# Kernel optimization log

Measured on AMD Instinct MI355X. Metric: run time of the kernel, lower is better.

## Reference

```python
import jax, jax.numpy as jnp
import numpy as np

N, T, D, E1 = 64, 32, 128, 128
EPS = 1e-6


def _mlp(x, W1, b1, W2, b2):
    # Linear -> ReLU -> (Dropout: identity in eval) -> Linear
    return jnp.maximum(x @ W1 + b1, 0.0) @ W2 + b2


def _forward(x_time, x_news,
             it_W1, it_b1, it_W2, it_b2,
             inw_W1, inw_b1, inw_W2, inw_b2,
             t2n_W1, t2n_b1, t2n_W2, t2n_b2,
             n2t_W1, n2t_b1, n2t_W2, n2t_b2,
             f_W1, f_b1, f_W2, f_b2,
             theta_t, theta_n):
    xt = x_time.reshape(-1, D)   # [NT, D]
    xn = x_news.reshape(-1, D)   # [NT, D]

    # incidence-matrix candidates, each [NT, E1]
    H_time = xt @ _mlp(xt.T, it_W1, it_b1, it_W2, it_b2)
    H_news = xn @ _mlp(xn.T, inw_W1, inw_b1, inw_W2, inw_b2)
    H_t2n = xt @ _mlp(xn.T, t2n_W1, t2n_b1, t2n_W2, t2n_b2)
    H_n2t = xn @ _mlp(xt.T, n2t_W1, n2t_b1, n2t_W2, n2t_b2)

    H = _mlp(jnp.concatenate([H_time, H_news, H_t2n, H_n2t], axis=1),
             f_W1, f_b1, f_W2, f_b2)  # [NT, E1]

    # column-wise standardization (torch.std is unbiased -> ddof=1) + softmax over nodes
    H = (H - H.mean(axis=0, keepdims=True)) / (H.std(axis=0, ddof=1, keepdims=True) + EPS)
    H = jax.nn.softmax(H, axis=0)

    # pairwise Jensen-Shannon divergence between columns of H -> [E1, E1]
    logH = jnp.log(H)
    M = (H[:, :, None] + H[:, None, :]) * 0.5          # [NT, E1, E1]
    kl_pm = jnp.sum(H[:, :, None] * (logH[:, :, None] - jnp.log(M)), axis=0)  # KL(P||M)
    # KL(Q||M)[i,j] == KL(P||M)[j,i] since M is symmetric in (i,j)
    jsd = (kl_pm + kl_pm.T) * 0.5

    jm = jsd.mean(axis=0)                               # [E1]
    njm = (jm - jm.mean()) / (jm.std(ddof=1) + EPS)
    w = jax.nn.softmax(njm)                             # diagonal of hyperedge weight W

    # Hypergraph conv with residual: x + elu(H @ diag(w) @ H.T @ x @ theta)
    # reassociated (exactly equal math) to avoid the O((NT)^2) intermediate
    Hw = H * w[None, :]                                 # [NT, E1]
    xt = xt + jax.nn.elu(Hw @ (H.T @ (xt @ theta_t)))
    xn = xn + jax.nn.elu(Hw @ (H.T @ (xn @ theta_n)))

    return xt.reshape(N, T, D), xn.reshape(N, T, D)


def setup_inputs() -> dict:
    key = jax.random.key(0)
    ks = iter(jax.random.split(key, 32))
    NT = N * T

    def lin(i, o):
        return (jax.random.normal(next(ks), (i, o), jnp.float32) / np.float32(np.sqrt(i)))

    inp = {
        "x_time": jax.random.normal(next(ks), (N, T, D), jnp.float32),
        "x_news": jax.random.normal(next(ks), (N, T, D), jnp.float32),
    }
    for pre in ["it", "inw", "t2n", "n2t"]:
        inp[pre + "_W1"] = lin(NT, E1)
        inp[pre + "_b1"] = jnp.zeros((E1,), jnp.float32)
        inp[pre + "_W2"] = lin(E1, E1)
        inp[pre + "_b2"] = jnp.zeros((E1,), jnp.float32)
    inp["f_W1"] = lin(4 * E1, E1)
    inp["f_b1"] = jnp.zeros((E1,), jnp.float32)
    inp["f_W2"] = lin(E1, E1)
    inp["f_b2"] = jnp.zeros((E1,), jnp.float32)
    # HypergraphConvolution uses torch.randn init for theta
    inp["theta_t"] = jax.random.normal(next(ks), (D, D), jnp.float32)
    inp["theta_n"] = jax.random.normal(next(ks), (D, D), jnp.float32)
    return inp


def reference(x_time, x_news,
              it_W1, it_b1, it_W2, it_b2,
              inw_W1, inw_b1, inw_W2, inw_b2,
              t2n_W1, t2n_b1, t2n_W2, t2n_b2,
              n2t_W1, n2t_b1, n2t_W2, n2t_b2,
              f_W1, f_b1, f_W2, f_b2,
              theta_t, theta_n):
    return _forward(x_time, x_news,
                    it_W1, it_b1, it_W2, it_b2,
                    inw_W1, inw_b1, inw_W2, inw_b2,
                    t2n_W1, t2n_b1, t2n_W2, t2n_b2,
                    n2t_W1, n2t_b1, n2t_W2, n2t_b2,
                    f_W1, f_b1, f_W2, f_b2,
                    theta_t, theta_n)
```

## Files before the change

kernel.cpp:

```cpp
#include <hip/hip_runtime.h>
#include <hip/hip_bf16.h>
#include <math.h>

#define NTOT 2048
#define DIM  128
#define MSPLIT 16
#define ZSPLIT 16
#define JT 16
#define JNC 128
#define JNSPLIT 16

struct P4 { const float* p[4]; };

__global__ __launch_bounds__(256) void gk_mlp1t(P4 X, P4 W1, float* __restrict__ Gs) {
  int k = blockIdx.z;
  int m0 = (blockIdx.x & 3) * 32;
  int e0 = (blockIdx.x >> 2) * 32;
  int split = blockIdx.y;
  int n0 = split * (NTOT / MSPLIT);
  const float* Xp = X.p[k];
  const float* Wp = W1.p[k];
  __shared__ float Xs[32][36], Ws[32][36];
  int tid = threadIdx.x;
  int lr = tid >> 3;
  int lc = (tid & 7) * 4;
  int tx = tid & 15, ty = tid >> 4;
  float a00 = 0.f, a01 = 0.f, a10 = 0.f, a11 = 0.f;
  long g0 = (long)(n0 + lr) * DIM;
  float4 xv = *(const float4*)(Xp + g0 + m0 + lc);
  float4 wv = *(const float4*)(Wp + g0 + e0 + lc);
  for (int nb = 0; nb < NTOT / MSPLIT; nb += 32) {
    *(float4*)&Xs[lr][lc] = xv;
    *(float4*)&Ws[lr][lc] = wv;
    __syncthreads();
    if (nb + 32 < NTOT / MSPLIT) {
      long gn = (long)(n0 + nb + 32 + lr) * DIM;
      xv = *(const float4*)(Xp + gn + m0 + lc);
      wv = *(const float4*)(Wp + gn + e0 + lc);
    }
    #pragma unroll
    for (int nn = 0; nn < 32; ++nn) {
      float x0 = Xs[nn][2*ty], x1 = Xs[nn][2*ty+1];
      float w0 = Ws[nn][2*tx], w1 = Ws[nn][2*tx+1];
      a00 += x0 * w0; a01 += x0 * w1;
      a10 += x1 * w0; a11 += x1 * w1;
    }
    __syncthreads();
  }
  float* Gk = Gs + ((long)k * MSPLIT + split) * 16384;
  int m = m0 + 2 * ty, e = e0 + 2 * tx;
  Gk[m * DIM + e]           = a00;
  Gk[m * DIM + e + 1]       = a01;
  Gk[(m + 1) * DIM + e]     = a10;
  Gk[(m + 1) * DIM + e + 1] = a11;
}

__global__ __launch_bounds__(256) void gk_mab(const float* __restrict__ Gs, P4 B1, P4 W2, P4 B2,
                                              const float* __restrict__ fW1, float* __restrict__ AB) {
  int m = blockIdx.x;
  int e = threadIdx.x & 127;
  int half = threadIdx.x >> 7;
  int k0 = half, k1 = half + 2;
  __shared__ float rk[4][DIM];
  __shared__ float mk[4][DIM];
  {
    const float* G0 = Gs + (long)k0 * MSPLIT * 16384 + m * DIM + e;
    const float* G1 = Gs + (long)k1 * MSPLIT * 16384 + m * DIM + e;
    float s0 = 0.f, s1 = 0.f;
    #pragma unroll
    for (int s = 0; s < MSPLIT; ++s) { s0 += G0[s * 16384]; s1 += G1[s * 16384]; }
    rk[k0][e] = fmaxf(s0 + B1.p[k0][e], 0.f);
    rk[k1][e] = fmaxf(s1 + B1.p[k1][e], 0.f);
  }
  __syncthreads();
  {
    const float* Wa = W2.p[k0];
    const float* Wb = W2.p[k1];
    float a0 = B2.p[k0][e], a1 = B2.p[k1][e];
    #pragma unroll 8
    for (int j = 0; j < DIM; ++j) {
      a0 += rk[k0][j] * Wa[j * DIM + e];
      a1 += rk[k1][j] * Wb[j * DIM + e];
    }
    mk[k0][e] = a0;
    mk[k1][e] = a1;
  }
  __syncthreads();
  const float* Ma = mk[half];
  const float* Mb = mk[half + 2];
  const float* W0 = fW1 + (half == 0 ? 0 : 128) * DIM;
  const float* W1p = fW1 + (half == 0 ? 256 : 384) * DIM;
  float acc = 0.f;
  #pragma unroll 8
  for (int j = 0; j < DIM; ++j)
    acc += Ma[j] * W0[j * DIM + e] + Mb[j] * W1p[j * DIM + e];
  AB[(long)half * 16384 + m * DIM + e] = acc;
}

__global__ __launch_bounds__(256) void gk_h12t(const float* __restrict__ xt, const float* __restrict__ xn,
                                               const float* __restrict__ AB, const float* __restrict__ fb1,
                                               const float* __restrict__ fW2, const float* __restrict__ fb2,
                                               float* __restrict__ HrawT) {
  int n0 = blockIdx.x * 8;
  int e  = threadIdx.x & 127;
  int rr = (threadIdx.x >> 7) << 2;
  __shared__ float stT[DIM][8], snT[DIM][8], h1T[DIM][8];
  {
    int c = threadIdx.x & 31, rq = threadIdx.x >> 5;
    const float* xtr = xt + (long)(n0 + rq) * DIM;
    const float* xnr = xn + (long)(n0 + rq) * DIM;
    #pragma unroll
    for (int i = 0; i < 4; ++i) {
      int d = c + 32 * i;
      stT[d][rq] = xtr[d];
      snT[d][rq] = xnr[d];
    }
  }
  __syncthreads();
  float4 acc1 = make_float4(0.f, 0.f, 0.f, 0.f);
  #pragma unroll 8
  for (int k = 0; k < DIM; ++k) {
    float a = AB[k * DIM + e];
    float b = AB[16384 + k * DIM + e];
    const float4 xv = *(const float4*)&stT[k][rr];
    const float4 nv = *(const float4*)&snT[k][rr];
    acc1.x += xv.x * a + nv.x * b;
    acc1.y += xv.y * a + nv.y * b;
    acc1.z += xv.z * a + nv.z * b;
    acc1.w += xv.w * a + nv.w * b;
  }
  float b1v = fb1[e];
  float4 h1;
  h1.x = fmaxf(acc1.x + b1v, 0.f);
  h1.y = fmaxf(acc1.y + b1v, 0.f);
  h1.z = fmaxf(acc1.z + b1v, 0.f);
  h1.w = fmaxf(acc1.w + b1v, 0.f);
  *(float4*)&h1T[e][rr] = h1;
  __syncthreads();
  float4 acc2 = make_float4(0.f, 0.f, 0.f, 0.f);
  #pragma unroll 8
  for (int j = 0; j < DIM; ++j) {
    float wv = fW2[j * DIM + e];
    const float4 hv = *(const float4*)&h1T[j][rr];
    acc2.x += hv.x * wv;
    acc2.y += hv.y * wv;
    acc2.z += hv.z * wv;
    acc2.w += hv.w * wv;
  }
  float b2v = fb2[e];
  float4 o;
  o.x = acc2.x + b2v; o.y = acc2.y + b2v; o.z = acc2.z + b2v; o.w = acc2.w + b2v;
  *(float4*)&HrawT[(long)e * NTOT + n0 + rr] = o;
}

__global__ __launch_bounds__(256) void colsoft_k(const float* __restrict__ HrawT,
                                                 float* __restrict__ HTp, float* __restrict__ Ecol,
                                                 float* __restrict__ Gacc) {
  int e = blockIdx.x;
  int t = threadIdx.x;
  if (e == 0 && t < DIM) Gacc[t] = 0.f;
  __shared__ float sa[4], sb[4], sc[4];
  float v[8];
  float sum = 0.f, sq = 0.f, mx = -3.4e38f;
  #pragma unroll
  for (int r = 0; r < 8; ++r) {
    float x = HrawT[(long)e * NTOT + t + 256 * r];
    v[r] = x;
    sum += x; sq += x * x; mx = fmaxf(mx, x);
  }
  #pragma unroll
  for (int o = 32; o > 0; o >>= 1) {
    sum += __shfl_down(sum, o);
    sq  += __shfl_down(sq, o);
    mx   = fmaxf(mx, __shfl_down(mx, o));
  }
  if ((t & 63) == 0) { int w = t >> 6; sa[w] = sum; sb[w] = sq; sc[w] = mx; }
  __syncthreads();
  sum = sa[0] + sa[1] + sa[2] + sa[3];
  sq  = sb[0] + sb[1] + sb[2] + sb[3];
  mx  = fmaxf(fmaxf(sc[0], sc[1]), fmaxf(sc[2], sc[3]));
  float mean = sum * (1.f / NTOT);
  float var  = (sq - sum * mean) * (1.f / (NTOT - 1));
  float ia   = 1.f / (sqrtf(fmaxf(var, 0.f)) + 1e-6f);
  float smax = (mx - mean) * ia;
  __syncthreads();

  float den = 0.f;
  #pragma unroll
  for (int r = 0; r < 8; ++r) {
    float s = (v[r] - mean) * ia - smax;
    v[r] = s;
    den += __expf(s);
  }
  #pragma unroll
  for (int o = 32; o > 0; o >>= 1) den += __shfl_down(den, o);
  if ((t & 63) == 0) sa[t >> 6] = den;
  __syncthreads();
  den = sa[0] + sa[1] + sa[2] + sa[3];
  float logden = __logf(den);
  float invden = 1.f / den;
  __syncthreads();

  float ent = 0.f;
  #pragma unroll
  for (int r = 0; r < 8; ++r) {
    float s = v[r];
    float pv = __expf(s) * invden;
    HTp[(long)e * NTOT + t + 256 * r] = pv;
    ent += pv * (s - logden);
  }
  #pragma unroll
  for (int o = 32; o > 0; o >>= 1) ent += __shfl_down(ent, o);
  if ((t & 63) == 0) sa[t >> 6] = ent;
  __syncthreads();
  if (t == 0) Ecol[e] = sa[0] + sa[1] + sa[2] + sa[3];
}

__global__ __launch_bounds__(256) void jx_k(const float* __restrict__ HTp,
                                            const float* __restrict__ xt, const float* __restrict__ xn,
                                            float* __restrict__ g, float* __restrict__ Xzs) {
  __shared__ union {
    struct { float Ti[JT][JNC + 2], Tj[JT][JNC + 2], red[JT][JT + 1]; } j;
    struct { float As[32][33], Bs[32][36]; } x;
  } sm;
  int bid = blockIdx.x;
  int tid = threadIdx.x;

  if (bid < 576) {
    int ny = bid / 36, b = bid - ny * 36;
    int bi = 0, rem = b;
    while (rem >= 8 - bi) { rem -= 8 - bi; ++bi; }
    int bj = bi + rem;
    int n0 = ny * (NTOT / JNSPLIT);
    int ti = tid >> 4, tj = tid & 15;
    bool active = (bi != bj) || (ti < tj);
    int lc = tid >> 4, ln = (tid & 15) * 8;
    const float* si = HTp + (long)(bi * JT + lc) * NTOT + n0 + ln;
    const float* sj = HTp + (long)(bj * JT + lc) * NTOT + n0 + ln;
    #pragma unroll
    for (int r = 0; r < 8; ++r) sm.j.Ti[lc][ln + r] = si[r];
    #pragma unroll
    for (int r = 0; r < 8; ++r) sm.j.Tj[lc][ln + r] = sj[r];
    __syncthreads();
    float acc = 0.f;
    if (active) {
      #pragma unroll 4
      for (int n = 0; n < JNC; ++n) {
        float s = sm.j.Ti[ti][n] + sm.j.Tj[tj][n];
        acc += s * __logf(fmaxf(0.5f * s, 1e-38f));
      }
    }
    sm.j.red[ti][tj] = active ? acc : 0.f;
    __syncthreads();
    if (tid < JT) {
      float s = 0.f;
      #pragma unroll
      for (int q = 0; q < JT; ++q) s += sm.j.red[tid][q];
      atomicAdd(&g[bi * JT + tid], -s);
    } else if (tid < 2 * JT) {
      int c2 = tid - JT;
      float s = 0.f;
      #pragma unroll
      for (int i = 0; i < JT; ++i) s += sm.j.red[i][c2];
      atomicAdd(&g[bj * JT + c2], -s);
    }
  } else {
    int id = bid - 576;
    int bt = id >> 8;
    int split = (id >> 4) & 15;
    int t16 = id & 15;
    const float* x = bt ? xn : xt;
    float* C = Xzs + ((long)bt * ZSPLIT + split) * 16384;
    int e0 = (t16 & 3) * 32, d0 = (t16 >> 2) * 32;
    int n0 = split * (NTOT / ZSPLIT);
    int col = tid & 31, row = tid >> 5;
    int lr = tid >> 3, lc4 = (tid & 7) * 4;
    int tx = tid & 15, ty = tid >> 4;
    float a00 = 0.f, a01 = 0.f, a10 = 0.f, a11 = 0.f;
    float pa[4]; float4 pb;
    #pragma unroll
    for (int r = 0; r < 4; ++r) pa[r] = HTp[(long)(e0 + row + r * 8) * NTOT + n0 + col];
    pb = *(const float4*)(x + (long)(n0 + lr) * DIM + d0 + lc4);
    for (int nb = 0; nb < NTOT / ZSPLIT; nb += 32) {
      #pragma unroll
      for (int r = 0; r < 4; ++r) sm.x.As[col][row + r * 8] = pa[r];
      *(float4*)&sm.x.Bs[lr][lc4] = pb;
      __syncthreads();
      if (nb + 32 < NTOT / ZSPLIT) {
        #pragma unroll
        for (int r = 0; r < 4; ++r)
          pa[r] = HTp[(long)(e0 + row + r * 8) * NTOT + n0 + nb + 32 + col];
        pb = *(const float4*)(x + (long)(n0 + nb + 32 + lr) * DIM + d0 + lc4);
      }
      #pragma unroll
      for (int nn = 0; nn < 32; ++nn) {
        float e0v = sm.x.As[nn][2*ty], e1v = sm.x.As[nn][2*ty+1];
        float d0v = sm.x.Bs[nn][2*tx], d1v = sm.x.Bs[nn][2*tx+1];
        a00 += e0v * d0v; a01 += e0v * d1v;
        a10 += e1v * d0v; a11 += e1v * d1v;
      }
      __syncthreads();
    }
    int e = e0 + 2 * ty, d = d0 + 2 * tx;
    C[e * DIM + d]           = a00;
    C[e * DIM + d + 1]       = a01;
    C[(e + 1) * DIM + d]     = a10;
    C[(e + 1) * DIM + d + 1] = a11;
  }
}

__global__ __launch_bounds__(128) void zs_k(const float* __restrict__ Xzs, const float* __restrict__ thT,
                                            const float* __restrict__ thN, const float* __restrict__ g,
                                            const float* __restrict__ Ecol, float* __restrict__ Zw) {
  int e = blockIdx.x, d = threadIdx.x, bt = blockIdx.y;
  float we;
  {
    int l = threadIdx.x & 63;
    float gA = g[l], gB = g[l + 64];
    float eA = Ecol[l], eB = Ecol[l + 64];
    float S = eA + eB;
    #pragma unroll
    for (int o = 32; o > 0; o >>= 1) S += __shfl_xor(S, o);
    float jA = (gA + 126.f * eA + S) * (1.f / 256.f);
    float jB = (gB + 126.f * eB + S) * (1.f / 256.f);
    float sn = jA + jB;
    #pragma unroll
    for (int o = 32; o > 0; o >>= 1) sn += __shfl_xor(sn, o);
    float mean = sn * (1.f / 128.f);
    float dA = jA - mean, dB = jB - mean;
    float q = dA * dA + dB * dB;
    #pragma unroll
    for (int o = 32; o > 0; o >>= 1) q += __shfl_xor(q, o);
    float inv = 1.f / (sqrtf(q * (1.f / 127.f)) + 1e-6f);
    float nA = dA * inv, nB = dB * inv;
    float mx = fmaxf(nA, nB);
    #pragma unroll
    for (int o = 32; o > 0; o >>= 1) mx = fmaxf(mx, __shfl_xor(mx, o));
    float xA = __expf(nA - mx), xB = __expf(nB - mx);
    float den = xA + xB;
    #pragma unroll
    for (int o = 32; o > 0; o >>= 1) den += __shfl_xor(den, o);
    float sel = (e < 64) ? nA : nB;
    float ne = __shfl(sel, e & 63);
    we = __expf(ne - mx) / den;
  }
  const float* src = Xzs + (long)bt * ZSPLIT * 16384 + e * DIM + d;
  const float* th = bt ? thN : thT;
  __shared__ float s[DIM];
  float xv = 0.f;
  #pragma unroll
  for (int sp = 0; sp < ZSPLIT; ++sp) xv += src[sp * 16384];
  s[d] = xv;
  __syncthreads();
  float acc = 0.f;
  #pragma unroll 8
  for (int k = 0; k < DIM; ++k) acc += s[k] * th[(long)k * DIM + d];
  Zw[bt * 16384 + e * DIM + d] = acc * we;
}

__global__ __launch_bounds__(256) void uk_t(const float* __restrict__ HTp, const float* __restrict__ Zw,
                                            const float* __restrict__ xt, const float* __restrict__ xn,
                                            float* __restrict__ out) {
  int bt = blockIdx.z;
  const float* x = bt ? xn : xt;
  const float* B = Zw + bt * 16384;
  float* o = out + (long)bt * NTOT * DIM;
  int d0 = blockIdx.x * 32, n0 = blockIdx.y * 32;
  __shared__ float As[32][33], Bs[32][36];
  int tid = threadIdx.x, col = tid & 31, row = tid >> 5;
  int lr = tid >> 3, lc4 = (tid & 7) * 4;
  int tx = tid & 15, ty = tid >> 4;
  float a00 = 0.f, a01 = 0.f, a10 = 0.f, a11 = 0.f;
  float pa[4]; float4 pb;
  #pragma unroll
  for (int r = 0; r < 4; ++r) pa[r] = HTp[(long)(row + r * 8) * NTOT + n0 + col];
  pb = *(const float4*)(B + (long)lr * DIM + d0 + lc4);
  for (int eb = 0; eb < DIM; eb += 32) {
    #pragma unroll
    for (int r = 0; r < 4; ++r) As[col][row + r * 8] = pa[r];
    *(float4*)&Bs[lr][lc4] = pb;
    __syncthreads();
    if (eb + 32 < DIM) {
      #pragma unroll
      for (int r = 0; r < 4; ++r)
        pa[r] = HTp[(long)(eb + 32 + row + r * 8) * NTOT + n0 + col];
      pb = *(const float4*)(B + (long)(eb + 32 + lr) * DIM + d0 + lc4);
    }
    #pragma unroll
    for (int ee = 0; ee < 32; ++ee) {
      float x0 = As[2*ty][ee], x1 = As[2*ty+1][ee];
      float b0 = Bs[ee][2*tx], b1 = Bs[ee][2*tx+1];
      a00 += x0 * b0; a01 += x0 * b1;
      a10 += x1 * b0; a11 += x1 * b1;
    }
    __syncthreads();
  }
  int n = n0 + 2 * ty, d = d0 + 2 * tx;
  long i0 = (long)n * DIM + d, i1 = i0 + DIM;
  float e00 = a00 > 0.f ? a00 : expm1f(a00);
  float e01 = a01 > 0.f ? a01 : expm1f(a01);
  float e10 = a10 > 0.f ? a10 : expm1f(a10);
  float e11 = a11 > 0.f ? a11 : expm1f(a11);
  o[i0]     = x[i0]     + e00;
  o[i0 + 1] = x[i0 + 1] + e01;
  o[i1]     = x[i1]     + e10;
  o[i1 + 1] = x[i1 + 1] + e11;
}

extern "C" void kernel_launch(void* const* d_in, const int* in_sizes, int n_in,
                              void* d_out, int out_size, void* d_ws, size_t ws_size,
                              hipStream_t stream) {
  const float* xt = (const float*)d_in[0];
  const float* xn = (const float*)d_in[1];
  const float *W1[4], *b1[4], *W2[4], *b2[4];
  for (int k = 0; k < 4; ++k) {
    W1[k] = (const float*)d_in[2 + 4*k];
    b1[k] = (const float*)d_in[3 + 4*k];
    W2[k] = (const float*)d_in[4 + 4*k];
    b2[k] = (const float*)d_in[5 + 4*k];
  }
  const float* fW1 = (const float*)d_in[18];
  const float* fb1 = (const float*)d_in[19];
  const float* fW2 = (const float*)d_in[20];
  const float* fb2 = (const float*)d_in[21];
  const float* thT = (const float*)d_in[22];
  const float* thN = (const float*)d_in[23];

  float* ws    = (float*)d_ws;
  float* Gacc  = ws;
  float* Ecol  = ws + 128;
  float* Zw    = ws + 384;
  float* Xzs   = ws + 33152;
  float* Gs    = ws + 557440;
  float* AB    = ws + 1606016;
  float* HrawT = ws + 1638784;
  float* HTp   = ws + 1900928;

  float* out = (float*)d_out;

  P4 Xs  = {{xt, xn, xn, xt}};
  P4 W1s = {{W1[0], W1[1], W1[2], W1[3]}};
  P4 B1s = {{b1[0], b1[1], b1[2], b1[3]}};
  P4 W2s = {{W2[0], W2[1], W2[2], W2[3]}};
  P4 B2s = {{b2[0], b2[1], b2[2], b2[3]}};

  gk_mlp1t<<<dim3(16, MSPLIT, 4), 256, 0, stream>>>(Xs, W1s, Gs);
  gk_mab  <<<128, 256, 0, stream>>>(Gs, B1s, W2s, B2s, fW1, AB);
  gk_h12t <<<256, 256, 0, stream>>>(xt, xn, AB, fb1, fW2, fb2, HrawT);

  colsoft_k<<<DIM, 256, 0, stream>>>(HrawT, HTp, Ecol, Gacc);

  jx_k<<<576 + 512, 256, 0, stream>>>(HTp, xt, xn, Gacc, Xzs);

  zs_k<<<dim3(128, 2), 128, 0, stream>>>(Xzs, thT, thN, Gacc, Ecol, Zw);
  uk_t<<<dim3(4, 64, 2), 256, 0, stream>>>(HTp, Zw, xt, xn, out);

  (void)in_sizes; (void)n_in; (void)out_size; (void)ws_size;
}
```

Before: 177.2 us.

## Use 64x64 register tiles with 4x4 per-thread outputs in GEMM kernels

The first-layer MLP GEMM and the H^T·x GEMM inside jx_k now use 64x64 output tiles, with each thread computing a 4x4 block from float4 shared-memory reads. This raises arithmetic intensity per shared-memory load. MSPLIT doubles so the MLP kernel keeps enough blocks, which doubles the partial-sum buffer and moves the workspace offsets. gk_h12t handles 4 rows per block instead of 8, doubling its grid for more parallelism at the cost of less reuse of the weight loads.

```diff
diff --git a/kernel.cpp b/kernel.cpp
--- a/kernel.cpp
+++ b/kernel.cpp
@@ -4,7 +4,7 @@
 
 #define NTOT 2048
 #define DIM  128
-#define MSPLIT 16
+#define MSPLIT 32
 #define ZSPLIT 16
 #define JT 16
 #define JNC 128
@@ -14,45 +14,53 @@
 
 __global__ __launch_bounds__(256) void gk_mlp1t(P4 X, P4 W1, float* __restrict__ Gs) {
   int k = blockIdx.z;
-  int m0 = (blockIdx.x & 3) * 32;
-  int e0 = (blockIdx.x >> 2) * 32;
+  int m0 = (blockIdx.x & 1) * 64;
+  int e0 = (blockIdx.x >> 1) * 64;
   int split = blockIdx.y;
   int n0 = split * (NTOT / MSPLIT);
   const float* Xp = X.p[k];
   const float* Wp = W1.p[k];
-  __shared__ float Xs[32][36], Ws[32][36];
+  __shared__ float Xs[32][68], Ws[32][68];
   int tid = threadIdx.x;
-  int lr = tid >> 3;
-  int lc = (tid & 7) * 4;
+  int lr = tid >> 4;
+  int lc = (tid & 15) * 4;
   int tx = tid & 15, ty = tid >> 4;
-  float a00 = 0.f, a01 = 0.f, a10 = 0.f, a11 = 0.f;
+  float4 acc0 = make_float4(0,0,0,0), acc1 = acc0, acc2 = acc0, acc3 = acc0;
   long g0 = (long)(n0 + lr) * DIM;
-  float4 xv = *(const float4*)(Xp + g0 + m0 + lc);
-  float4 wv = *(const float4*)(Wp + g0 + e0 + lc);
+  float4 px0 = *(const float4*)(Xp + g0 + m0 + lc);
+  float4 px1 = *(const float4*)(Xp + g0 + 16 * DIM + m0 + lc);
+  float4 pw0 = *(const float4*)(Wp + g0 + e0 + lc);
+  float4 pw1 = *(const float4*)(Wp + g0 + 16 * DIM + e0 + lc);
   for (int nb = 0; nb < NTOT / MSPLIT; nb += 32) {
-    *(float4*)&Xs[lr][lc] = xv;
-    *(float4*)&Ws[lr][lc] = wv;
+    *(float4*)&Xs[lr][lc]      = px0;
+    *(float4*)&Xs[lr + 16][lc] = px1;
+    *(float4*)&Ws[lr][lc]      = pw0;
+    *(float4*)&Ws[lr + 16][lc] = pw1;
     __syncthreads();
     if (nb + 32 < NTOT / MSPLIT) {
       long gn = (long)(n0 + nb + 32 + lr) * DIM;
-      xv = *(const float4*)(Xp + gn + m0 + lc);
-      wv = *(const float4*)(Wp + gn + e0 + lc);
+      px0 = *(const float4*)(Xp + gn + m0 + lc);
+      px1 = *(const float4*)(Xp + gn + 16 * DIM + m0 + lc);
+      pw0 = *(const float4*)(Wp + gn + e0 + lc);
+      pw1 = *(const float4*)(Wp + gn + 16 * DIM + e0 + lc);
     }
     #pragma unroll
     for (int nn = 0; nn < 32; ++nn) {
-      float x0 = Xs[nn][2*ty], x1 = Xs[nn][2*ty+1];
-      float w0 = Ws[nn][2*tx], w1 = Ws[nn][2*tx+1];
-      a00 += x0 * w0; a01 += x0 * w1;
-      a10 += x1 * w0; a11 += x1 * w1;
+      float4 a = *(const float4*)&Xs[nn][4 * ty];
+      float4 b = *(const float4*)&Ws[nn][4 * tx];
+      acc0.x += a.x*b.x; acc0.y += a.x*b.y; acc0.z += a.x*b.z; acc0.w += a.x*b.w;
+      acc1.x += a.y*b.x; acc1.y += a.y*b.y; acc1.z += a.y*b.z; acc1.w += a.y*b.w;
+      acc2.x += a.z*b.x; acc2.y += a.z*b.y; acc2.z += a.z*b.z; acc2.w += a.z*b.w;
+      acc3.x += a.w*b.x; acc3.y += a.w*b.y; acc3.z += a.w*b.z; acc3.w += a.w*b.w;
     }
     __syncthreads();
   }
   float* Gk = Gs + ((long)k * MSPLIT + split) * 16384;
-  int m = m0 + 2 * ty, e = e0 + 2 * tx;
-  Gk[m * DIM + e]           = a00;
-  Gk[m * DIM + e + 1]       = a01;
-  Gk[(m + 1) * DIM + e]     = a10;
-  Gk[(m + 1) * DIM + e + 1] = a11;
+  int m = m0 + 4 * ty, e = e0 + 4 * tx;
+  *(float4*)(Gk + (m + 0) * DIM + e) = acc0;
+  *(float4*)(Gk + (m + 1) * DIM + e) = acc1;
+  *(float4*)(Gk + (m + 2) * DIM + e) = acc2;
+  *(float4*)(Gk + (m + 3) * DIM + e) = acc3;
 }
 
 __global__ __launch_bounds__(256) void gk_mab(const float* __restrict__ Gs, P4 B1, P4 W2, P4 B2,
@@ -101,56 +109,48 @@
                                                const float* __restrict__ AB, const float* __restrict__ fb1,
                                                const float* __restrict__ fW2, const float* __restrict__ fb2,
                                                float* __restrict__ HrawT) {
-  int n0 = blockIdx.x * 8;
+  int n0 = blockIdx.x * 4;
   int e  = threadIdx.x & 127;
-  int rr = (threadIdx.x >> 7) << 2;
-  __shared__ float stT[DIM][8], snT[DIM][8], h1T[DIM][8];
+  int half = threadIdx.x >> 7;
+  __shared__ float xT[DIM][4], nT[DIM][4], h1T[DIM][4];
   {
     int c = threadIdx.x & 31, rq = threadIdx.x >> 5;
-    const float* xtr = xt + (long)(n0 + rq) * DIM;
-    const float* xnr = xn + (long)(n0 + rq) * DIM;
+    const float* src = (rq < 4) ? (xt + (long)(n0 + rq) * DIM)
+                                : (xn + (long)(n0 + rq - 4) * DIM);
+    float (*dst)[4] = (rq < 4) ? xT : nT;
+    int rr = rq & 3;
     #pragma unroll
     for (int i = 0; i < 4; ++i) {
       int d = c + 32 * i;
-      stT[d][rq] = xtr[d];
-      snT[d][rq] = xnr[d];
-    }
-  }
-  __syncthreads();
-  float4 acc1 = make_float4(0.f, 0.f, 0.f, 0.f);
+      dst[d][rr] = src[d];
+    }
+  }
+  __syncthreads();
+  float2 acc1 = make_float2(0.f, 0.f);
   #pragma unroll 8
   for (int k = 0; k < DIM; ++k) {
     float a = AB[k * DIM + e];
     float b = AB[16384 + k * DIM + e];
-    const float4 xv = *(const float4*)&stT[k][rr];
-    const float4 nv = *(const float4*)&snT[k][rr];
+    float2 xv = *(const float2*)&xT[k][half * 2];
+    float2 nv = *(const float2*)&nT[k][half * 2];
     acc1.x += xv.x * a + nv.x * b;
     acc1.y += xv.y * a + nv.y * b;
-    acc1.z += xv.z * a + nv.z * b;
-    acc1.w += xv.w * a + nv.w * b;
   }
   float b1v = fb1[e];
-  float4 h1;
-  h1.x = fmaxf(acc1.x + b1v, 0.f);
-  h1.y = fmaxf(acc1.y + b1v, 0.f);
-  h1.z = fmaxf(acc1.z + b1v, 0.f);
-  h1.w = fmaxf(acc1.w + b1v, 0.f);
-  *(float4*)&h1T[e][rr] = h1;
-  __syncthreads();
-  float4 acc2 = make_float4(0.f, 0.f, 0.f, 0.f);
+  float2 h1 = make_float2(fmaxf(acc1.x + b1v, 0.f), fmaxf(acc1.y + b1v, 0.f));
+  *(float2*)&h1T[e][half * 2] = h1;
+  __syncthreads();
+  float2 acc2 = make_float2(0.f, 0.f);
   #pragma unroll 8
   for (int j = 0; j < DIM; ++j) {
     float wv = fW2[j * DIM + e];
-    const float4 hv = *(const float4*)&h1T[j][rr];
+    float2 hv = *(const float2*)&h1T[j][half * 2];
     acc2.x += hv.x * wv;
     acc2.y += hv.y * wv;
-    acc2.z += hv.z * wv;
-    acc2.w += hv.w * wv;
   }
   float b2v = fb2[e];
-  float4 o;
-  o.x = acc2.x + b2v; o.y = acc2.y + b2v; o.z = acc2.z + b2v; o.w = acc2.w + b2v;
-  *(float4*)&HrawT[(long)e * NTOT + n0 + rr] = o;
+  float2 o = make_float2(acc2.x + b2v, acc2.y + b2v);
+  *(float2*)&HrawT[(long)e * NTOT + n0 + half * 2] = o;
 }
 
 __global__ __launch_bounds__(256) void colsoft_k(const float* __restrict__ HrawT,
@@ -221,7 +221,7 @@
                                             float* __restrict__ g, float* __restrict__ Xzs) {
   __shared__ union {
     struct { float Ti[JT][JNC + 2], Tj[JT][JNC + 2], red[JT][JT + 1]; } j;
-    struct { float As[32][33], Bs[32][36]; } x;
+    struct { float As[32][68], Bs[32][68]; } x;
   } sm;
   int bid = blockIdx.x;
   int tid = threadIdx.x;
@@ -266,46 +266,51 @@
     }
   } else {
     int id = bid - 576;
-    int bt = id >> 8;
-    int split = (id >> 4) & 15;
-    int t16 = id & 15;
+    int bt = id >> 6;
+    int split = (id >> 2) & 15;
+    int t4 = id & 3;
+    int e0 = (t4 & 1) * 64, d0 = (t4 >> 1) * 64;
+    int n0 = split * (NTOT / ZSPLIT);
     const float* x = bt ? xn : xt;
     float* C = Xzs + ((long)bt * ZSPLIT + split) * 16384;
-    int e0 = (t16 & 3) * 32, d0 = (t16 >> 2) * 32;
-    int n0 = split * (NTOT / ZSPLIT);
-    int col = tid & 31, row = tid >> 5;
-    int lr = tid >> 3, lc4 = (tid & 7) * 4;
+    int col = tid & 31, er = tid >> 5;
+    int lr = tid >> 4, lc = (tid & 15) * 4;
     int tx = tid & 15, ty = tid >> 4;
-    float a00 = 0.f, a01 = 0.f, a10 = 0.f, a11 = 0.f;
-    float pa[4]; float4 pb;
-    #pragma unroll
-    for (int r = 0; r < 4; ++r) pa[r] = HTp[(long)(e0 + row + r * 8) * NTOT + n0 + col];
-    pb = *(const float4*)(x + (long)(n0 + lr) * DIM + d0 + lc4);
+    float4 acc0 = make_float4(0,0,0,0), acc1 = acc0, acc2 = acc0, acc3 = acc0;
+    float pa[8]; float4 pb0, pb1;
+    #pragma unroll
+    for (int r = 0; r < 8; ++r) pa[r] = HTp[(long)(e0 + er + 8 * r) * NTOT + n0 + col];
+    pb0 = *(const float4*)(x + (long)(n0 + lr) * DIM + d0 + lc);
+    pb1 = *(const float4*)(x + (long)(n0 + lr + 16) * DIM + d0 + lc);
     for (int nb = 0; nb < NTOT / ZSPLIT; nb += 32) {
       #pragma unroll
-      for (int r = 0; r < 4; ++r) sm.x.As[col][row + r * 8] = pa[r];
-      *(float4*)&sm.x.Bs[lr][lc4] = pb;
+      for (int r = 0; r < 8; ++r) sm.x.As[col][er + 8 * r] = pa[r];
+      *(float4*)&sm.x.Bs[lr][lc]      = pb0;
+      *(float4*)&sm.x.Bs[lr + 16][lc] = pb1;
       __syncthreads();
       if (nb + 32 < NTOT / ZSPLIT) {
         #pragma unroll
-        for (int r = 0; r < 4; ++r)
-          pa[r] = HTp[(long)(e0 + row + r * 8) * NTOT + n0 + nb + 32 + col];
-        pb = *(const float4*)(x + (long)(n0 + nb + 32 + lr) * DIM + d0 + lc4);
+        for (int r = 0; r < 8; ++r)
+          pa[r] = HTp[(long)(e0 + er + 8 * r) * NTOT + n0 + nb + 32 + col];
+        pb0 = *(const float4*)(x + (long)(n0 + nb + 32 + lr) * DIM + d0 + lc);
+        pb1 = *(const float4*)(x + (long)(n0 + nb + 48 + lr) * DIM + d0 + lc);
       }
       #pragma unroll
       for (int nn = 0; nn < 32; ++nn) {
-        float e0v = sm.x.As[nn][2*ty], e1v = sm.x.As[nn][2*ty+1];
-        float d0v = sm.x.Bs[nn][2*tx], d1v = sm.x.Bs[nn][2*tx+1];
-        a00 += e0v * d0v; a01 += e0v * d1v;
-        a10 += e1v * d0v; a11 += e1v * d1v;
+        float4 a = *(const float4*)&sm.x.As[nn][4 * ty];
+        float4 b = *(const float4*)&sm.x.Bs[nn][4 * tx];
+        acc0.x += a.x*b.x; acc0.y += a.x*b.y; acc0.z += a.x*b.z; acc0.w += a.x*b.w;
+        acc1.x += a.y*b.x; acc1.y += a.y*b.y; acc1.z += a.y*b.z; acc1.w += a.y*b.w;
+        acc2.x += a.z*b.x; acc2.y += a.z*b.y; acc2.z += a.z*b.z; acc2.w += a.z*b.w;
+        acc3.x += a.w*b.x; acc3.y += a.w*b.y; acc3.z += a.w*b.z; acc3.w += a.w*b.w;
       }
       __syncthreads();
     }
-    int e = e0 + 2 * ty, d = d0 + 2 * tx;
-    C[e * DIM + d]           = a00;
-    C[e * DIM + d + 1]       = a01;
-    C[(e + 1) * DIM + d]     = a10;
-    C[(e + 1) * DIM + d + 1] = a11;
+    int e = e0 + 4 * ty, d = d0 + 4 * tx;
+    *(float4*)(C + (e + 0) * DIM + d) = acc0;
+    *(float4*)(C + (e + 1) * DIM + d) = acc1;
+    *(float4*)(C + (e + 2) * DIM + d) = acc2;
+    *(float4*)(C + (e + 3) * DIM + d) = acc3;
   }
 }
 
@@ -432,9 +437,9 @@
   float* Zw    = ws + 384;
   float* Xzs   = ws + 33152;
   float* Gs    = ws + 557440;
-  float* AB    = ws + 1606016;
-  float* HrawT = ws + 1638784;
-  float* HTp   = ws + 1900928;
+  float* AB    = ws + 2654592;
+  float* HrawT = ws + 2687360;
+  float* HTp   = ws + 2949504;
 
   float* out = (float*)d_out;
 
@@ -444,13 +449,13 @@
   P4 W2s = {{W2[0], W2[1], W2[2], W2[3]}};
   P4 B2s = {{b2[0], b2[1], b2[2], b2[3]}};
 
-  gk_mlp1t<<<dim3(16, MSPLIT, 4), 256, 0, stream>>>(Xs, W1s, Gs);
+  gk_mlp1t<<<dim3(4, MSPLIT, 4), 256, 0, stream>>>(Xs, W1s, Gs);
   gk_mab  <<<128, 256, 0, stream>>>(Gs, B1s, W2s, B2s, fW1, AB);
-  gk_h12t <<<256, 256, 0, stream>>>(xt, xn, AB, fb1, fW2, fb2, HrawT);
+  gk_h12t <<<512, 256, 0, stream>>>(xt, xn, AB, fb1, fW2, fb2, HrawT);
 
   colsoft_k<<<DIM, 256, 0, stream>>>(HrawT, HTp, Ecol, Gacc);
 
-  jx_k<<<576 + 512, 256, 0, stream>>>(HTp, xt, xn, Gacc, Xzs);
+  jx_k<<<576 + 128, 256, 0, stream>>>(HTp, xt, xn, Gacc, Xzs);
 
   zs_k<<<dim3(128, 2), 128, 0, stream>>>(Xzs, thT, thN, Gacc, Ecol, Zw);
   uk_t<<<dim3(4, 64, 2), 256, 0, stream>>>(HTp, Zw, xt, xn, out);
```

Measured after the change: 189.0 us. +6.7%, slower.
